# Kernel tuning notes

Hardware: AMD Instinct MI355X
Metric: run time of the kernel (lower is better)

The kernel has to match this reference:

```python
import jax, jax.numpy as jnp
from jax import lax
import numpy as np

B, S, D, H = 64, 512, 1024, 1024


def setup_inputs() -> dict:
    key = jax.random.key(0)
    ks = jax.random.split(key, 9)
    s = 1.0 / np.sqrt(H)
    return {
        "x": jax.random.normal(ks[0], (B, S, D), jnp.float32),
        "W_ih0": jax.random.normal(ks[1], (H, D), jnp.float32) * s,
        "b_ih0": jax.random.normal(ks[2], (H,), jnp.float32) * s,
        "W_hh0": jax.random.normal(ks[3], (H, H), jnp.float32) * s,
        "b_hh0": jax.random.normal(ks[4], (H,), jnp.float32) * s,
        "W_ih1": jax.random.normal(ks[5], (H, H), jnp.float32) * s,
        "b_ih1": jax.random.normal(ks[6], (H,), jnp.float32) * s,
        "W_hh1": jax.random.normal(ks[7], (H, H), jnp.float32) * s,
        "b_hh1": jax.random.normal(ks[8], (H,), jnp.float32) * s,
    }


def reference(x, W_ih0, b_ih0, W_hh0, b_hh0, W_ih1, b_ih1, W_hh1, b_hh1):
    batch = x.shape[0]
    hid = W_hh0.shape[0]
    params = [(W_ih0, b_ih0, W_hh0, b_hh0), (W_ih1, b_ih1, W_hh1, b_hh1)]
    h0 = jnp.zeros((len(params), batch, hid), x.dtype)

    def step(h, xt):
        # xt: [B, D]; h: [L, B, H]
        inp = xt
        new_h = []
        for l, (Wi, bi, Wh, bh) in enumerate(params):
            inp = jnp.tanh(inp @ Wi.T + bi + h[l] @ Wh.T + bh)
            new_h.append(inp)
        return jnp.stack(new_h), inp

    hT, outs = lax.scan(step, h0, jnp.swapaxes(x, 0, 1))  # outs: [S, B, H]
    return jnp.swapaxes(outs, 0, 1), hT
```

## Files before the change

kernel.cpp:

```cpp
#include <hip/hip_runtime.h>
#include <hip/hip_bf16.h>

#define RNN_B 64
#define RNN_S 512
#define RNN_H 1024
#define BH (RNN_B * RNN_H)
#define L0_NBLK 64
#define L1_NBLK 128
#define NBLK (L0_NBLK + L1_NBLK)
#define NFLAGS 192
#define FLAG_STRIDE 32
#define OUTS_ELEMS ((size_t)RNN_B * RNN_S * RNN_H)

typedef _Float16 f16;
typedef __attribute__((ext_vector_type(8))) _Float16 f16x8;
typedef __attribute__((ext_vector_type(8))) short bf16x8;
typedef __attribute__((ext_vector_type(4))) float f32x4;
typedef __attribute__((ext_vector_type(4))) int i32x4;

__device__ f32x4 __rnn_rawbufload_x4(i32x4 srsrc, int voffset, int soffset,
                                     int cachepolicy) __asm("llvm.amdgcn.raw.buffer.load.v4f32");

__device__ __forceinline__ i32x4 make_srd(const void* p, unsigned bytes) {
  i32x4 r;
  r[0] = (int)(unsigned)(unsigned long long)p;
  r[1] = (int)((unsigned long long)p >> 32);
  r[2] = (int)bytes;
  r[3] = 0x00020000;
  return r;
}

__device__ __forceinline__ f16x8 ld_h(i32x4 srd, int byteoff) {
  union { f32x4 f; f16x8 h; } u;
  u.f = __rnn_rawbufload_x4(srd, byteoff, 0, 17);
  return u.h;
}

__device__ __forceinline__ void st_sys_u16(void* p, unsigned v) {
  asm volatile("global_store_short %0, %1, off sc0 sc1" :: "v"(p), "v"(v) : "memory");
}

__device__ __forceinline__ unsigned f16bits(float f) {
  union { f16 h; unsigned short u; } v; v.h = (f16)f; return (unsigned)v.u;
}
__device__ __forceinline__ short f2bf(float f) {
  union { float f; unsigned u; } v; v.f = f;
  return (short)((v.u + 0x7FFFu + ((v.u >> 16) & 1u)) >> 16);
}
__device__ __forceinline__ float bf2f(short h) {
  union { unsigned u; float f; } v; v.u = ((unsigned)(unsigned short)h) << 16;
  return v.f;
}
__device__ __forceinline__ f32x4 mfma16b(bf16x8 a, bf16x8 b, f32x4 c) {
  return __builtin_amdgcn_mfma_f32_16x16x32_bf16(a, b, c, 0, 0, 0);
}
__device__ __forceinline__ f32x4 mfma16f(f16x8 a, f16x8 b, f32x4 c) {
  return __builtin_amdgcn_mfma_f32_16x16x32_f16(a, b, c, 0, 0, 0);
}
__device__ __forceinline__ void cvt8_hl(const float* f, bf16x8* hi, bf16x8* lo) {
  #pragma unroll
  for (int i = 0; i < 8; ++i) {
    short h = f2bf(f[i]);
    (*hi)[i] = h;
    (*lo)[i] = f2bf(f[i] - bf2f(h));
  }
}
__device__ __forceinline__ f16x8 cvt8f(const float* f) {
  f16x8 r;
  #pragma unroll
  for (int i = 0; i < 8; ++i) r[i] = (f16)f[i];
  return r;
}

__global__ __launch_bounds__(256) void a0_gemm(
    const float* __restrict__ x, const float* __restrict__ Wih0,
    const float* __restrict__ bih0, const float* __restrict__ bhh0,
    float* __restrict__ A0, unsigned* __restrict__ flags)
{
  if (blockIdx.x == 0) {
    for (int i = threadIdx.x; i < NFLAGS * FLAG_STRIDE; i += 256)
      __hip_atomic_store(&flags[i], 0u, __ATOMIC_RELAXED, __HIP_MEMORY_SCOPE_SYSTEM);
  }
  const int bn = blockIdx.x & 7;
  const int bm = blockIdx.x >> 3;
  const int tid = threadIdx.x;
  const int lane = tid & 63;
  const int w = tid >> 6;
  const int wr = w >> 1, wc = w & 1;
  const int l15 = lane & 15, lq = lane >> 4;

  __shared__ short As[2][128][40];
  __shared__ short Bs[2][128][40];

  f32x4 acc[4][4] = {};

  const int sr = tid >> 1;
  const int sc = (tid & 1) << 4;
  const float* xp = x + (size_t)(bm * 128 + sr) * RNN_H + sc;
  const float* wp = Wih0 + (size_t)(bn * 128 + sr) * RNN_H + sc;

  for (int k0 = 0; k0 < RNN_H; k0 += 32) {
    float xa[16], wa[16];
    #pragma unroll
    for (int j = 0; j < 4; ++j) {
      *(float4*)&xa[j * 4] = *(const float4*)(xp + k0 + j * 4);
      *(float4*)&wa[j * 4] = *(const float4*)(wp + k0 + j * 4);
    }
    __syncthreads();
    bf16x8 h0, l0, h1, l1;
    cvt8_hl(&xa[0], &h0, &l0); cvt8_hl(&xa[8], &h1, &l1);
    *(bf16x8*)&As[0][sr][sc] = h0; *(bf16x8*)&As[1][sr][sc] = l0;
    *(bf16x8*)&As[0][sr][sc + 8] = h1; *(bf16x8*)&As[1][sr][sc + 8] = l1;
    cvt8_hl(&wa[0], &h0, &l0); cvt8_hl(&wa[8], &h1, &l1);
    *(bf16x8*)&Bs[0][sr][sc] = h0; *(bf16x8*)&Bs[1][sr][sc] = l0;
    *(bf16x8*)&Bs[0][sr][sc + 8] = h1; *(bf16x8*)&Bs[1][sr][sc + 8] = l1;
    __syncthreads();
    bf16x8 ah[4], al[4], bh[4], bl[4];
    #pragma unroll
    for (int i = 0; i < 4; ++i) {
      ah[i] = *(const bf16x8*)&As[0][wr * 64 + i * 16 + l15][lq * 8];
      al[i] = *(const bf16x8*)&As[1][wr * 64 + i * 16 + l15][lq * 8];
    }
    #pragma unroll
    for (int j = 0; j < 4; ++j) {
      bh[j] = *(const bf16x8*)&Bs[0][wc * 64 + j * 16 + l15][lq * 8];
      bl[j] = *(const bf16x8*)&Bs[1][wc * 64 + j * 16 + l15][lq * 8];
    }
    #pragma unroll
    for (int i = 0; i < 4; ++i)
      #pragma unroll
      for (int j = 0; j < 4; ++j) {
        acc[i][j] = mfma16b(ah[i], bh[j], acc[i][j]);
        acc[i][j] = mfma16b(al[i], bh[j], acc[i][j]);
        acc[i][j] = mfma16b(ah[i], bl[j], acc[i][j]);
      }
  }

  #pragma unroll
  for (int j = 0; j < 4; ++j) {
    const int col = bn * 128 + wc * 64 + j * 16 + l15;
    const float bias = bih0[col] + bhh0[col];
    #pragma unroll
    for (int i = 0; i < 4; ++i) {
      const int row0 = bm * 128 + wr * 64 + i * 16 + lq * 4;
      #pragma unroll
      for (int r = 0; r < 4; ++r)
        A0[(size_t)(row0 + r) * RNN_H + col] = acc[i][j][r] + bias;
    }
  }
}

__device__ __forceinline__ void waitflags(const unsigned* fbase, int tL0, int tL1) {
  if (threadIdx.x < 64) {
    const int l = threadIdx.x;
    const unsigned* f = fbase + (l < 48 ? l : 0) * FLAG_STRIDE;
    const int tgt = (l < 16) ? tL0 : (l < 48 ? tL1 : 0);
    while (!__all((int)__hip_atomic_load(f, __ATOMIC_RELAXED,
                                         __HIP_MEMORY_SCOPE_SYSTEM) >= tgt))
      __builtin_amdgcn_s_sleep(1);
  }
  __syncthreads();
}

__device__ __forceinline__ void publish(unsigned* slot, unsigned v) {
  asm volatile("s_waitcnt vmcnt(0)" ::: "memory");
  __syncthreads();
  if (threadIdx.x == 0)
    __hip_atomic_store(slot, v, __ATOMIC_RELAXED, __HIP_MEMORY_SCOPE_SYSTEM);
}

__global__ __launch_bounds__(256) void rnn_rec(
    const float* __restrict__ Whh0,
    const float* __restrict__ Wih1, const float* __restrict__ bih1,
    const float* __restrict__ Whh1, const float* __restrict__ bhh1,
    float* outs,
    f16* __restrict__ h0buf,
    f16* __restrict__ h1buf,
    unsigned* flags, int dmask)
{
  const int bid = blockIdx.x;
  const bool isL0 = bid < L0_NBLK;
  const int tid = threadIdx.x;
  const int w = tid >> 6;
  const int lane = tid & 63;
  const int l15 = lane & 15;
  const int lq = lane >> 4;
  const int swz = l15 & 7;
  const int dlag = dmask;

  int b0, n0, bs, cs;
  if (isL0) { bs = bid >> 4; cs = bid & 15; b0 = bs * 16; n0 = cs * 64; }
  else { const int b2 = bid - L0_NBLK; bs = b2 >> 5; cs = b2 & 31; b0 = bs * 16; n0 = cs * 32; }

  unsigned* fbase = flags + bs * 48 * FLAG_STRIDE;
  unsigned* myflag = fbase + (isL0 ? cs : 16 + cs) * FLAG_STRIDE;

  const unsigned HBYT = (unsigned)(dmask + 1) * BH * 2u;
  const i32x4 srd_h0 = make_srd(h0buf, HBYT);
  const i32x4 srd_h1 = make_srd(h1buf, HBYT);

  __shared__ __align__(16) f16 Ws[2 * 32 * RNN_H];
  __shared__ float red[4][16][64];

  if (isL0) {
    const int n = tid >> 2;
    const int kb = (tid & 3) * 256;
    const float* src = Whh0 + (size_t)(n0 + n) * RNN_H + kb;
    f16* dst = Ws + n * RNN_H;
    #pragma unroll 4
    for (int j = 0; j < 32; ++j) {
      float tmp[8];
      *(float4*)&tmp[0] = *(const float4*)(src + j * 8);
      *(float4*)&tmp[4] = *(const float4*)(src + j * 8 + 4);
      const int c = (kb >> 3) + j;
      *(f16x8*)&dst[((c ^ (n & 7)) << 3)] = cvt8f(tmp);
    }
  } else {
    const int n = tid >> 3;
    const int kb = (tid & 7) * 128;
    #pragma unroll
    for (int m = 0; m < 2; ++m) {
      const float* src = (m ? Whh1 : Wih1) + (size_t)(n0 + n) * RNN_H + kb;
      f16* dst = Ws + m * 32 * RNN_H + n * RNN_H;
      #pragma unroll 4
      for (int j = 0; j < 16; ++j) {
        float tmp[8];
        *(float4*)&tmp[0] = *(const float4*)(src + j * 8);
        *(float4*)&tmp[4] = *(const float4*)(src + j * 8 + 4);
        const int c = (kb >> 3) + j;
        *(f16x8*)&dst[((c ^ (n & 7)) << 3)] = cvt8f(tmp);
      }
    }
  }

  float* hT = outs + OUTS_ELEMS;

  int ccol, crg;
  float bias1s = 0.f;
  if (isL0) { ccol = tid & 63; crg = tid >> 6; }
  else      { ccol = tid & 31; crg = tid >> 5;
              bias1s = bih1[n0 + ccol] + bhh1[n0 + ccol]; }
  __syncthreads();

  if (isL0) {
    float a0v[4];
    #pragma unroll
    for (int r = 0; r < 4; ++r)
      a0v[r] = outs[((size_t)(b0 + crg * 4 + r) * RNN_S + 0) * RNN_H + n0 + ccol];

    for (int p = 0; p < RNN_S; ++p) {
      waitflags(fbase, p, p - dlag);
      if (p > 0) {
        const int hb = (((p - 1) & dmask) * BH + (b0 + l15) * RNN_H + w * 256 + lq * 8) * 2;
        f32x4 acc[4] = {};
        #pragma unroll
        for (int ks = 0; ks < 8; ++ks) {
          f16x8 hx = ld_h(srd_h0, hb + ks * 64);
          const int c = ((w * 32 + ks * 4 + lq) ^ swz) << 3;
          #pragma unroll
          for (int ct = 0; ct < 4; ++ct)
            acc[ct] = mfma16f(hx, *(const f16x8*)&Ws[(ct * 16 + l15) * RNN_H + c], acc[ct]);
        }
        #pragma unroll
        for (int ct = 0; ct < 4; ++ct)
          #pragma unroll
          for (int r = 0; r < 4; ++r)
            red[w][lq * 4 + r][ct * 16 + l15] = acc[ct][r];
      }
      __syncthreads();
      float vals[4];
      #pragma unroll
      for (int r = 0; r < 4; ++r) {
        const int row = crg * 4 + r;
        float s = a0v[r];
        if (p > 0)
          s += red[0][row][ccol] + red[1][row][ccol] + red[2][row][ccol] + red[3][row][ccol];
        vals[r] = tanhf(s);
        st_sys_u16(&h0buf[(size_t)(p & dmask) * BH + (size_t)(b0 + row) * RNN_H + n0 + ccol],
                   f16bits(vals[r]));
      }
      if (p == RNN_S - 1) {
        #pragma unroll
        for (int r = 0; r < 4; ++r)
          hT[(size_t)(b0 + crg * 4 + r) * RNN_H + n0 + ccol] = vals[r];
      }
      if (p + 1 < RNN_S) {
        #pragma unroll
        for (int r = 0; r < 4; ++r)
          a0v[r] = outs[((size_t)(b0 + crg * 4 + r) * RNN_S + (p + 1)) * RNN_H + n0 + ccol];
      }
      publish(myflag, (unsigned)(p + 1));
    }
  } else {
    for (int t = 0; t < RNN_S; ++t) {
      waitflags(fbase, t + 1, t);
      const int hb0 = ((t & dmask) * BH + (b0 + l15) * RNN_H + w * 256 + lq * 8) * 2;
      f32x4 acc[2] = {};
      if (t > 0) {
        const int hb1 = (((t - 1) & dmask) * BH + (b0 + l15) * RNN_H + w * 256 + lq * 8) * 2;
        #pragma unroll
        for (int ks = 0; ks < 8; ++ks) {
          f16x8 hx = ld_h(srd_h0, hb0 + ks * 64);
          f16x8 gx = ld_h(srd_h1, hb1 + ks * 64);
          const int c = ((w * 32 + ks * 4 + lq) ^ swz) << 3;
          #pragma unroll
          for (int ct = 0; ct < 2; ++ct) {
            acc[ct] = mfma16f(hx, *(const f16x8*)&Ws[(ct * 16 + l15) * RNN_H + c], acc[ct]);
            acc[ct] = mfma16f(gx, *(const f16x8*)&Ws[32 * RNN_H + (ct * 16 + l15) * RNN_H + c], acc[ct]);
          }
        }
      } else {
        #pragma unroll
        for (int ks = 0; ks < 8; ++ks) {
          f16x8 hx = ld_h(srd_h0, hb0 + ks * 64);
          const int c = ((w * 32 + ks * 4 + lq) ^ swz) << 3;
          #pragma unroll
          for (int ct = 0; ct < 2; ++ct)
            acc[ct] = mfma16f(hx, *(const f16x8*)&Ws[(ct * 16 + l15) * RNN_H + c], acc[ct]);
        }
      }
      #pragma unroll
      for (int ct = 0; ct < 2; ++ct)
        #pragma unroll
        for (int r = 0; r < 4; ++r)
          red[w][lq * 4 + r][ct * 16 + l15] = acc[ct][r];
      __syncthreads();
      #pragma unroll
      for (int r = 0; r < 2; ++r) {
        const int row = crg * 2 + r;
        float s = bias1s + red[0][row][ccol] + red[1][row][ccol]
                         + red[2][row][ccol] + red[3][row][ccol];
        const float v = tanhf(s);
        st_sys_u16(&h1buf[(size_t)(t & dmask) * BH + (size_t)(b0 + row) * RNN_H + n0 + ccol],
                   f16bits(v));
        outs[((size_t)(b0 + row) * RNN_S + t) * RNN_H + n0 + ccol] = v;
        if (t == RNN_S - 1)
          hT[(size_t)BH + (size_t)(b0 + row) * RNN_H + n0 + ccol] = v;
      }
      publish(myflag, (unsigned)(t + 1));
    }
  }
}

extern "C" void kernel_launch(void* const* d_in, const int* in_sizes, int n_in,
                              void* d_out, int out_size, void* d_ws, size_t ws_size,
                              hipStream_t stream) {
  const float* x    = (const float*)d_in[0];
  const float* Wih0 = (const float*)d_in[1];
  const float* bih0 = (const float*)d_in[2];
  const float* Whh0 = (const float*)d_in[3];
  const float* bhh0 = (const float*)d_in[4];
  const float* Wih1 = (const float*)d_in[5];
  const float* bih1 = (const float*)d_in[6];
  const float* Whh1 = (const float*)d_in[7];
  const float* bhh1 = (const float*)d_in[8];
  float* outs = (float*)d_out;

  const size_t flagBytes = 32768;
  const size_t need4 = flagBytes + 2 * (size_t)4 * BH * sizeof(f16);
  const int D = (ws_size >= need4) ? 4 : 2;
  unsigned* flags = (unsigned*)d_ws;
  f16* h0buf = (f16*)((char*)d_ws + flagBytes);
  f16* h1buf = h0buf + (size_t)D * BH;

  a0_gemm<<<2048, 256, 0, stream>>>(x, Wih0, bih0, bhh0, outs, flags);
  rnn_rec<<<NBLK, 256, 0, stream>>>(Whh0, Wih1, bih1, Whh1, bhh1, outs,
                                    h0buf, h1buf, flags, D - 1);
}
```

Baseline: 2.611 ms.

## Replace per-block flags with per-domain atomic counters and publish earlier

Per-block step flags are replaced by two atomic counters per batch slice, one per layer. Each block increments its counter with fetch_add, and waiters poll just two lanes against scaled targets instead of 48 flags. The publish is moved before the outs/hT/next-A0 loads and stores, so consumers are released as soon as the h buffer is written and the non-critical global writes are taken off the critical path. The cost is atomic contention on a shared counter, and a single counter per layer means blocks further ahead can make the count look complete while a lagging block's data is not yet written.

After: 2.940 ms. +12.6%, slower.

```diff
diff --git a/kernel.cpp b/kernel.cpp
--- a/kernel.cpp
+++ b/kernel.cpp
@@ -8,7 +8,6 @@
 #define L0_NBLK 64
 #define L1_NBLK 128
 #define NBLK (L0_NBLK + L1_NBLK)
-#define NFLAGS 192
 #define FLAG_STRIDE 32
 #define OUTS_ELEMS ((size_t)RNN_B * RNN_S * RNN_H)
 
@@ -78,7 +77,7 @@
     float* __restrict__ A0, unsigned* __restrict__ flags)
 {
   if (blockIdx.x == 0) {
-    for (int i = threadIdx.x; i < NFLAGS * FLAG_STRIDE; i += 256)
+    for (int i = threadIdx.x; i < 8 * FLAG_STRIDE; i += 256)
       __hip_atomic_store(&flags[i], 0u, __ATOMIC_RELAXED, __HIP_MEMORY_SCOPE_SYSTEM);
   }
   const int bn = blockIdx.x & 7;
@@ -150,11 +149,11 @@
   }
 }
 
-__device__ __forceinline__ void waitflags(const unsigned* fbase, int tL0, int tL1) {
+__device__ __forceinline__ void waitcnt2(const unsigned* fdom, int tL0, int tL1) {
   if (threadIdx.x < 64) {
     const int l = threadIdx.x;
-    const unsigned* f = fbase + (l < 48 ? l : 0) * FLAG_STRIDE;
-    const int tgt = (l < 16) ? tL0 : (l < 48 ? tL1 : 0);
+    const unsigned* f = fdom + (l == 1 ? FLAG_STRIDE : 0);
+    const int tgt = (l == 0) ? tL0 : (l == 1 ? tL1 : (-0x7FFFFFFF));
     while (!__all((int)__hip_atomic_load(f, __ATOMIC_RELAXED,
                                          __HIP_MEMORY_SCOPE_SYSTEM) >= tgt))
       __builtin_amdgcn_s_sleep(1);
@@ -162,11 +161,11 @@
   __syncthreads();
 }
 
-__device__ __forceinline__ void publish(unsigned* slot, unsigned v) {
+__device__ __forceinline__ void publish(unsigned* cnt) {
   asm volatile("s_waitcnt vmcnt(0)" ::: "memory");
   __syncthreads();
   if (threadIdx.x == 0)
-    __hip_atomic_store(slot, v, __ATOMIC_RELAXED, __HIP_MEMORY_SCOPE_SYSTEM);
+    __hip_atomic_fetch_add(cnt, 1u, __ATOMIC_RELAXED, __HIP_MEMORY_SCOPE_SYSTEM);
 }
 
 __global__ __launch_bounds__(256) void rnn_rec(
@@ -192,8 +191,8 @@
   if (isL0) { bs = bid >> 4; cs = bid & 15; b0 = bs * 16; n0 = cs * 64; }
   else { const int b2 = bid - L0_NBLK; bs = b2 >> 5; cs = b2 & 31; b0 = bs * 16; n0 = cs * 32; }
 
-  unsigned* fbase = flags + bs * 48 * FLAG_STRIDE;
-  unsigned* myflag = fbase + (isL0 ? cs : 16 + cs) * FLAG_STRIDE;
+  unsigned* fdom = flags + bs * 2 * FLAG_STRIDE;
+  unsigned* mycnt = fdom + (isL0 ? 0 : FLAG_STRIDE);
 
   const unsigned HBYT = (unsigned)(dmask + 1) * BH * 2u;
   const i32x4 srd_h0 = make_srd(h0buf, HBYT);
@@ -249,7 +248,7 @@
       a0v[r] = outs[((size_t)(b0 + crg * 4 + r) * RNN_S + 0) * RNN_H + n0 + ccol];
 
     for (int p = 0; p < RNN_S; ++p) {
-      waitflags(fbase, p, p - dlag);
+      waitcnt2(fdom, 16 * p, 32 * (p - dlag));
       if (p > 0) {
         const int hb = (((p - 1) & dmask) * BH + (b0 + l15) * RNN_H + w * 256 + lq * 8) * 2;
         f32x4 acc[4] = {};
@@ -279,6 +278,7 @@
         st_sys_u16(&h0buf[(size_t)(p & dmask) * BH + (size_t)(b0 + row) * RNN_H + n0 + ccol],
                    f16bits(vals[r]));
       }
+      publish(mycnt);
       if (p == RNN_S - 1) {
         #pragma unroll
         for (int r = 0; r < 4; ++r)
@@ -289,11 +289,10 @@
         for (int r = 0; r < 4; ++r)
           a0v[r] = outs[((size_t)(b0 + crg * 4 + r) * RNN_S + (p + 1)) * RNN_H + n0 + ccol];
       }
-      publish(myflag, (unsigned)(p + 1));
     }
   } else {
     for (int t = 0; t < RNN_S; ++t) {
-      waitflags(fbase, t + 1, t);
+      waitcnt2(fdom, 16 * (t + 1), 32 * t);
       const int hb0 = ((t & dmask) * BH + (b0 + l15) * RNN_H + w * 256 + lq * 8) * 2;
       f32x4 acc[2] = {};
       if (t > 0) {
@@ -325,19 +324,24 @@
         for (int r = 0; r < 4; ++r)
           red[w][lq * 4 + r][ct * 16 + l15] = acc[ct][r];
       __syncthreads();
+      float v2[2];
       #pragma unroll
       for (int r = 0; r < 2; ++r) {
         const int row = crg * 2 + r;
         float s = bias1s + red[0][row][ccol] + red[1][row][ccol]
                          + red[2][row][ccol] + red[3][row][ccol];
-        const float v = tanhf(s);
+        v2[r] = tanhf(s);
         st_sys_u16(&h1buf[(size_t)(t & dmask) * BH + (size_t)(b0 + row) * RNN_H + n0 + ccol],
-                   f16bits(v));
-        outs[((size_t)(b0 + row) * RNN_S + t) * RNN_H + n0 + ccol] = v;
+                   f16bits(v2[r]));
+      }
+      publish(mycnt);
+      #pragma unroll
+      for (int r = 0; r < 2; ++r) {
+        const int row = crg * 2 + r;
+        outs[((size_t)(b0 + row) * RNN_S + t) * RNN_H + n0 + ccol] = v2[r];
         if (t == RNN_S - 1)
-          hT[(size_t)BH + (size_t)(b0 + row) * RNN_H + n0 + ccol] = v;
-      }
-      publish(myflag, (unsigned)(t + 1));
+          hT[(size_t)BH + (size_t)(b0 + row) * RNN_H + n0 + ccol] = v2[r];
+      }
     }
   }
 }
```
